# Kernel optimization log

Hardware: AMD Instinct MI355X
Metric: run time of the kernel (lower is better)

Reference implementation:

```python
import jax, jax.numpy as jnp
import numpy as np

KSIZE, SCALE, STRIDE, SOFTMAX_SCALE = 3, 3, 1, 10.0
ESCAPE_NAN = 1e-4
DN = ('NCHW', 'OIHW', 'NCHW')


def same_pad(x, k, stride):
    # torch same_padding: pad so out = ceil(in/stride)
    H, W = x.shape[-2], x.shape[-1]
    oh, ow = -(-H // stride), -(-W // stride)
    ph = max(0, (oh - 1) * stride + k - H)
    pw = max(0, (ow - 1) * stride + k - W)
    return jnp.pad(x, ((0, 0), (0, 0), (ph // 2, ph - ph // 2), (pw // 2, pw - pw // 2)))


def extract_patches(img, k, stride):
    # img [B,C,H,W] already padded -> [B, L, C, k, k], matching torch Unfold ordering (C slowest, kh, kw)
    B, C, H, W = img.shape
    oh, ow = (H - k) // stride + 1, (W - k) // stride + 1
    cols = [img[:, :, i:i + stride * oh:stride, j:j + stride * ow:stride]
            for i in range(k) for j in range(k)]
    p = jnp.stack(cols, axis=2)                      # [B, C, k*k, oh, ow]
    p = p.reshape(B, C, k, k, oh * ow)               # [B, C, k, k, L]
    return jnp.transpose(p, (0, 4, 1, 2, 3))         # [B, L, C, k, k]


def conv1x1_prelu(x, W, b, a):
    y = jnp.einsum('bchw,oc->bohw', x, W) + b[None, :, None, None]
    return jnp.where(y >= 0, y, a * y)


def bilinear_down(x, Ho, Wo):
    # F.interpolate(mode='bilinear', align_corners=False), no antialias
    H, W = x.shape[-2], x.shape[-1]
    def coords(o, s):
        src = (jnp.arange(o, dtype=jnp.float32) + 0.5) * (s / o) - 0.5
        src = jnp.clip(src, 0.0, s - 1.0)
        i0 = jnp.floor(src).astype(jnp.int32)
        i1 = jnp.minimum(i0 + 1, s - 1)
        return i0, i1, src - i0.astype(jnp.float32)
    y0, y1, wy = coords(Ho, H)
    x0, x1, wx = coords(Wo, W)
    r = x[:, :, y0, :] * (1.0 - wy)[:, None] + x[:, :, y1, :] * wy[:, None]
    return r[:, :, :, x0] * (1.0 - wx) + r[:, :, :, x1] * wx


def forward(x, Wa, ba, aa, Wm1, bm1, am1, Wm2, bm2, am2):
    B, C, H, W = x.shape
    kernel = SCALE * KSIZE  # 9
    embed_w = conv1x1_prelu(x, Wa, ba, aa)      # [B,C,H,W]
    match = conv1x1_prelu(x, Wm1, bm1, am1)     # [B,C/2,H,W]
    # large-scale patches used as conv_transpose kernels: [B, L, C, 9, 9]
    raw_w = extract_patches(same_pad(embed_w, kernel, STRIDE * SCALE), kernel, STRIDE * SCALE)
    Hr, Wr = H // SCALE, W // SCALE
    ref = conv1x1_prelu(bilinear_down(x, Hr, Wr), Wm2, bm2, am2)  # [B,C/2,Hr,Wr]
    # small-scale patches used as correlation kernels: [B, L, C/2, 3, 3]
    w = extract_patches(same_pad(ref, KSIZE, STRIDE), KSIZE, STRIDE)
    norm = jnp.sqrt(jnp.sum(w * w, axis=(2, 3, 4), keepdims=True))
    wn = w / jnp.maximum(norm, ESCAPE_NAN)
    xp = same_pad(match, KSIZE, 1)  # [B,C/2,H+2,W+2]

    def corr(xi, wi):  # xi [C/2,H+2,W+2], wi [L,C/2,3,3] -> [L,H,W]
        return jax.lax.conv_general_dilated(xi[None], wi, (1, 1), 'VALID', dimension_numbers=DN)[0]

    y = jax.vmap(corr)(xp, wn)                  # [B,L,H,W]
    y = jax.nn.softmax(y * SOFTMAX_SCALE, axis=1)

    pad = kernel - 1 - SCALE  # conv_transpose2d(stride=3, padding=3) equivalent padding = 5

    def tconv(yi, rwi):  # yi [L,H,W], rwi [L,C,9,9] -> [C,3H,3W]
        k = jnp.transpose(jnp.flip(rwi, (-2, -1)), (1, 0, 2, 3))  # [C,L,9,9]
        return jax.lax.conv_general_dilated(
            yi[None], k, (1, 1), [(pad, pad), (pad, pad)],
            lhs_dilation=(STRIDE * SCALE, STRIDE * SCALE), dimension_numbers=DN)[0]

    out = jax.vmap(tconv)(y, raw_w) / 6.0       # [B,C,3H,3W]
    return out


def setup_inputs() -> dict:
    key = jax.random.key(0)
    ks = jax.random.split(key, 8)
    B, C, H, W = 4, 64, 60, 60
    C2 = C // 2
    return {
        'x': jax.random.normal(ks[0], (B, C, H, W), jnp.float32),
        'Wa': jax.random.normal(ks[1], (C, C), jnp.float32) * 0.1,
        'ba': jax.random.normal(ks[2], (C,), jnp.float32) * 0.1,
        'aa': jnp.full((1,), 0.25, jnp.float32),
        'Wm1': jax.random.normal(ks[3], (C2, C), jnp.float32) * 0.1,
        'bm1': jax.random.normal(ks[4], (C2,), jnp.float32) * 0.1,
        'am1': jnp.full((1,), 0.25, jnp.float32),
        'Wm2': jax.random.normal(ks[5], (C2, C), jnp.float32) * 0.1,
        'bm2': jax.random.normal(ks[6], (C2,), jnp.float32) * 0.1,
        'am2': jnp.full((1,), 0.25, jnp.float32),
    }


def reference(x, Wa, ba, aa, Wm1, bm1, am1, Wm2, bm2, am2):
    return forward(x, Wa, ba, aa, Wm1, bm1, am1, Wm2, bm2, am2)
```

## Files before the change

### kernel.cpp

```cpp
#include <hip/hip_runtime.h>
#include <hip/hip_bf16.h>

typedef __hip_bfloat16 bf16_t;
using f32x4  = __attribute__((ext_vector_type(4))) float;
using bf16x8 = __attribute__((ext_vector_type(8))) short;

#define NB 4
#define NC 64
#define NC2 32
#define NH 60
#define NW 60
#define NPIX (NH*NW)
#define HP 66
#define MP 62
#define HR 20
#define RP 22
#define NL 400
#define OHW 180
#define KPAD 512

#define OFF_XPB   2230272
#define OFF_REFP  3214336
#define OFF_YBL   3462144
#define OFF_AP    14982144
#define OFF_EB    29727744
#define OFF_XP    32087040
#define OFF_RF    40381440

__global__ __launch_bounds__(256) void k_conv(
    const float* __restrict__ x,
    const float* __restrict__ Wa,  const float* __restrict__ ba,  const float* __restrict__ aa,
    const float* __restrict__ Wm1, const float* __restrict__ bm1, const float* __restrict__ am1,
    const float* __restrict__ Wm2, const float* __restrict__ bm2, const float* __restrict__ am2,
    bf16_t* __restrict__ E_bt, bf16_t* __restrict__ xpb, float* __restrict__ refp) {
  int bid = blockIdx.x;
  int t = threadIdx.x;
  if (bid < 300) {
    __shared__ float Ws[64*64];
    __shared__ float bs[64];
    __shared__ float al;
    int b = bid / 75, pblk = bid % 75;
    for (int i = t; i < 64*64; i += 256) {
      int co = i >> 6, c = i & 63;
      Ws[c*64 + co] = Wa[i];
    }
    if (t < 64) bs[t] = ba[t];
    if (t == 0) al = aa[0];
    __syncthreads();
    int lane = t & 63, wid = t >> 6;
    int pix0 = pblk*48 + wid*12;
    const float* xb = x + b*NC*NPIX + pix0;
    float acc[12];
    #pragma unroll
    for (int p = 0; p < 12; ++p) acc[p] = bs[lane];
    for (int c = 0; c < 64; ++c) {
      float wv = Ws[c*64 + lane];
      const float* xc = xb + c*NPIX;
      #pragma unroll
      for (int p = 0; p < 12; ++p)
        acc[p] = fmaf(xc[p], wv, acc[p]);
    }
    #pragma unroll
    for (int p = 0; p < 12; ++p) {
      float v = acc[p];
      v = v >= 0.f ? v : al*v;
      int pix = pix0 + p;
      int ph = pix / NW, pw = pix % NW;
      E_bt[((b*HP + ph+3)*HP + (pw+3))*NC + lane] = __float2bfloat16(v);
    }
  } else if (bid < 2100) {
    int idx = (bid - 300)*256 + t;
    int pix = idx % NPIX; int tmp = idx / NPIX;
    int co = tmp % NC2; int b = tmp / NC2;
    float alpha = am1[0];
    const float* xb = x + b*NC*NPIX + pix;
    const float* wr = Wm1 + co*64;
    float acc = bm1[co];
    #pragma unroll 8
    for (int c = 0; c < 64; ++c)
      acc = fmaf(xb[c*NPIX], wr[c], acc);
    acc = acc >= 0.f ? acc : alpha*acc;
    int ph = pix / NW, pw = pix % NW;
    xpb[((b*NC2 + co)*MP + ph+1)*MP + (pw+1)] = __float2bfloat16(acc);
  } else {
    int idx = (bid - 2100)*256 + t;
    int pos = idx % (HR*HR); int tmp = idx / (HR*HR);
    int co = tmp % NC2; int b = tmp / NC2;
    int hr = pos / HR, wr_ = pos % HR;
    float alpha = am2[0];
    const float* xb = x + b*NC*NPIX + (3*hr+1)*NW + (3*wr_+1);
    const float* wrow = Wm2 + co*64;
    float acc = bm2[co];
    #pragma unroll 8
    for (int c = 0; c < 64; ++c)
      acc = fmaf(xb[c*NPIX], wrow[c], acc);
    acc = acc >= 0.f ? acc : alpha*acc;
    refp[((b*NC2 + co)*RP + hr+1)*RP + (wr_+1)] = acc;
  }
}

__global__ __launch_bounds__(256) void k_swz(
    const bf16_t* __restrict__ xpb, const float* __restrict__ refp,
    const bf16_t* __restrict__ E_bt,
    bf16_t* __restrict__ Xp, bf16_t* __restrict__ Rf, bf16_t* __restrict__ Eb) {
  __shared__ float scl[16];
  int bid = blockIdx.x;
  int t = threadIdx.x;
  if (bid < 2025) {
    int tid = bid*256 + t;
    int slot = tid & 63; int rest = tid >> 6;
    int ks = rest % 9; int rest2 = rest / 9;
    int mblk = rest2 % 225; int b = rest2 / 225;
    int m = mblk*16 + (slot & 15);
    int h = m / NW, w = m % NW;
    int k0 = ks*32 + (slot >> 4)*8;
    const bf16_t* xb = xpb + (size_t)b*NC2*MP*MP;
    union { bf16_t a[8]; bf16x8 v; } u;
    #pragma unroll
    for (int j = 0; j < 8; ++j) {
      int k = k0 + j;
      int c = k / 9, r = k % 9;
      int i = r / 3, j2 = r % 3;
      u.a[j] = xb[(c*MP + h + i)*MP + w + j2];
    }
    *(bf16x8*)(Xp + (size_t)tid*8) = u.v;
  } else if (bid < 2125) {
    int r2 = bid - 2025;
    int nblk = r2 % 25, b = r2 / 25;
    int ll = t >> 4, sub = t & 15;
    int l = nblk*16 + ll;
    int lh = l / HR, lw = l % HR;
    const float* rb = refp + (size_t)b*NC2*RP*RP;
    float ss = 0.f;
    #pragma unroll
    for (int e0 = 0; e0 < 18; ++e0) {
      int e = sub*18 + e0;
      int c = e / 9, r = e % 9;
      int i = r / 3, j = r % 3;
      float v = rb[(c*RP + lh + i)*RP + lw + j];
      ss = fmaf(v, v, ss);
    }
    #pragma unroll
    for (int off = 1; off < 16; off <<= 1)
      ss += __shfl_xor(ss, off);
    if (sub == 0) scl[ll] = 10.f / fmaxf(sqrtf(ss), 1e-4f);
    __syncthreads();
    for (int sidx = t; sidx < 576; sidx += 256) {
      int ks = sidx >> 6, slot = sidx & 63;
      int l2 = nblk*16 + (slot & 15);
      int lh2 = l2 / HR, lw2 = l2 % HR;
      float sc = scl[slot & 15];
      int k0 = ks*32 + (slot >> 4)*8;
      union { bf16_t a[8]; bf16x8 v; } u;
      #pragma unroll
      for (int j = 0; j < 8; ++j) {
        int k = k0 + j;
        int c = k / 9, r = k % 9;
        int i = r / 3, j2 = r % 3;
        u.a[j] = __float2bfloat16(rb[(c*RP + lh2 + i)*RP + lw2 + j2] * sc);
      }
      *(bf16x8*)(Rf + ((size_t)(b*25 + nblk)*576 + sidx)*8) = u.v;
    }
  } else {
    int r2 = bid - 2125;
    int n = r2 % 576, b = r2 / 576;
    int c = n / 9, n9 = n % 9, rr = n9 / 3, s = n9 % 3;
    size_t nbase = ((size_t)(b*12 + n/48)*16);
    const unsigned short* Eu = (const unsigned short*)E_bt;
    unsigned short* Ebu = (unsigned short*)Eb;
    for (int k = t; k < KPAD; k += 256) {
      unsigned short v = 0;
      if (k < 484) {
        int u = k / 22, vv = k % 22;
        v = Eu[((size_t)((b*HP + 3*u + rr)*HP + 3*vv + s))*NC + c];
      }
      size_t idx = (((nbase + (k>>5))*3 + (n%48)/16)*64 + ((k>>3)&3)*16 + (n&15))*8 + (k&7);
      Ebu[idx] = v;
    }
  }
}

__global__ __launch_bounds__(64) void k_cgemm(
    const bf16x8* __restrict__ Xp, const bf16x8* __restrict__ Rf,
    bf16_t* __restrict__ y_bl) {
  int L = threadIdx.x;
  int o = blockIdx.x;
  int xcd = o & 7, sl = o >> 3;
  int w = (xcd < 4 ? xcd*188 : 752 + (xcd-4)*187) + sl;
  int b = w / 375; int rem = w % 375;
  int mt = rem / 5, nt = rem % 5;
  const bf16x8* pa = Xp + ((size_t)(b*225 + mt*3)*9)*64 + L;
  const bf16x8* pb = Rf + ((size_t)(b*25 + nt*5)*9)*64 + L;
  f32x4 acc[3][5];
  #pragma unroll
  for (int i = 0; i < 3; ++i)
    #pragma unroll
    for (int j = 0; j < 5; ++j)
      acc[i][j] = {0.f, 0.f, 0.f, 0.f};
  bf16x8 af[3], bf[5], afn[3], bfn[5];
  #pragma unroll
  for (int i = 0; i < 3; ++i) af[i] = pa[i*576];
  #pragma unroll
  for (int j = 0; j < 5; ++j) bf[j] = pb[j*576];
  for (int ks = 0; ks < 9; ++ks) {
    if (ks < 8) {
      #pragma unroll
      for (int i = 0; i < 3; ++i) afn[i] = pa[i*576 + (ks+1)*64];
      #pragma unroll
      for (int j = 0; j < 5; ++j) bfn[j] = pb[j*576 + (ks+1)*64];
    }
    #pragma unroll
    for (int i = 0; i < 3; ++i)
      #pragma unroll
      for (int j = 0; j < 5; ++j)
        acc[i][j] = __builtin_amdgcn_mfma_f32_16x16x32_bf16(af[i], bf[j], acc[i][j], 0, 0, 0);
    #pragma unroll
    for (int i = 0; i < 3; ++i) af[i] = afn[i];
    #pragma unroll
    for (int j = 0; j < 5; ++j) bf[j] = bfn[j];
  }
  int quad = L >> 4, col = L & 15;
  #pragma unroll
  for (int mf = 0; mf < 3; ++mf) {
    #pragma unroll
    for (int r = 0; r < 4; ++r) {
      int m = mt*48 + mf*16 + quad*4 + r;
      bf16_t* row = y_bl + ((size_t)(b*NPIX + m))*NL + nt*80 + col;
      #pragma unroll
      for (int nf = 0; nf < 5; ++nf)
        row[nf*16] = __float2bfloat16(acc[mf][nf][r]);
    }
  }
}

__device__ __forceinline__ float lo_bf(unsigned int u) {
  return __uint_as_float(u << 16);
}
__device__ __forceinline__ float hi_bf(unsigned int u) {
  return __uint_as_float(u & 0xffff0000u);
}
__device__ __forceinline__ float u16_bf(unsigned short u) {
  return __uint_as_float(((unsigned int)u) << 16);
}
__device__ __forceinline__ unsigned short bf_bits(float f) {
  union { bf16_t h; unsigned short u; } c;
  c.h = __float2bfloat16(f);
  return c.u;
}

__global__ __launch_bounds__(512) void k_saprime(
    const unsigned int* __restrict__ y_b32, bf16_t* __restrict__ Ap) {
  __shared__ uint4 raw[2592];
  unsigned short* ysp = (unsigned short*)raw;
  int t = threadIdx.x;
  int b = blockIdx.z;
  int h0base = blockIdx.y*4, w0base = blockIdx.x*4;
  for (int i = t; i < 2592; i += 512) raw[i] = uint4{0,0,0,0};
  __syncthreads();

  int wave = t >> 6, lane = t & 63;
  bool act = lane < 50;
  for (int pos = wave; pos < 36; pos += 8) {
    int i = pos / 6, jj = pos % 6;
    int hh = h0base - 1 + i, ww = w0base - 1 + jj;
    if (!((unsigned)hh < NH && (unsigned)ww < NW)) continue;
    const uint4* src4 = (const uint4*)(y_b32 + ((size_t)(b*NPIX + hh*NW + ww))*200);
    uint4 v = act ? src4[lane] : uint4{0,0,0,0};
    float f[8];
    if (act) {
      f[0] = lo_bf(v.x); f[1] = hi_bf(v.x);
      f[2] = lo_bf(v.y); f[3] = hi_bf(v.y);
      f[4] = lo_bf(v.z); f[5] = hi_bf(v.z);
      f[6] = lo_bf(v.w); f[7] = hi_bf(v.w);
    } else {
      #pragma unroll
      for (int k = 0; k < 8; ++k) f[k] = -1e30f;
    }
    float m = -1e30f;
    #pragma unroll
    for (int k = 0; k < 8; ++k) m = fmaxf(m, f[k]);
    #pragma unroll
    for (int off = 32; off > 0; off >>= 1)
      m = fmaxf(m, __shfl_xor(m, off));
    float s = 0.f;
    #pragma unroll
    for (int k = 0; k < 8; ++k) {
      float e = __expf(f[k] - m);
      f[k] = e;
      s += e;
    }
    #pragma unroll
    for (int off = 32; off > 0; off >>= 1)
      s += __shfl_xor(s, off);
    float r = 1.f / s;
    if (act) {
      #pragma unroll
      for (int k = 0; k < 4; ++k) {
        int l2 = lane*4 + k;
        int lh = l2 / 10, lw = 2*l2 - 20*lh;
        union { bf16_t h[2]; unsigned int u; } pk;
        pk.h[0] = __float2bfloat16(f[2*k]   * r);
        pk.h[1] = __float2bfloat16(f[2*k+1] * r);
        *(unsigned int*)&ysp[pos*576 + (lh+2)*24 + (lw+2)] = pk.u;
      }
    }
  }
  __syncthreads();

  int row = t >> 5;
  int klane = t & 31;
  int h0r = row >> 2, w0r = row & 3;
  int m = (h0base + h0r)*NW + (w0base + w0r);
  int pblk = m / 80, pf = (m % 80) >> 4, mrow = m & 15;
  size_t rowbase = ((size_t)(b*45 + pblk)*16);
  const unsigned short* basep = ysp + (h0r*6 + w0r)*576;
  unsigned short* Apu = (unsigned short*)Ap;
  for (int kk = 0; kk < 8; ++kk) {
    int k = kk*64 + 2*klane;
    float a0 = 0.f, a1 = 0.f;
    if (k < 484) {
      int u = k / 22, v = k - 22*u;
      const unsigned short* q = basep + u*24 + v;
      #pragma unroll
      for (int dh = 0; dh < 3; ++dh) {
        unsigned int p0 = *(const unsigned int*)(q + dh*3480);
        a0 += lo_bf(p0); a1 += hi_bf(p0);
        a0 += u16_bf(q[dh*3480 + 577]);
        a1 += u16_bf(q[dh*3480 + 578]);
        unsigned int p2 = *(const unsigned int*)(q + dh*3480 + 1154);
        a0 += lo_bf(p2); a1 += hi_bf(p2);
      }
    }
    unsigned int pk = ((unsigned int)bf_bits(a1) << 16) | bf_bits(a0);
    size_t idx = (((rowbase + (k>>5))*5 + pf)*64 + ((k>>3)&3)*16 + mrow)*8 + (k&7);
    *(unsigned int*)&Apu[idx] = pk;
  }
}

__global__ __launch_bounds__(64) void k_tgemm(
    const bf16x8* __restrict__ Eb, const bf16x8* __restrict__ Ap,
    float* __restrict__ out) {
  int L = threadIdx.x;
  int o = blockIdx.x;
  int w = (o & 7)*270 + (o >> 3);
  int b = w / 540; int rem = w % 540;
  int pbi = rem / 12, rb = rem % 12;
  const bf16x8* pa = Eb + ((size_t)(b*12 + rb)*16)*3*64 + L;
  const bf16x8* pp = Ap + ((size_t)(b*45 + pbi)*16)*5*64 + L;
  f32x4 acc[3][5];
  #pragma unroll
  for (int i = 0; i < 3; ++i)
    #pragma unroll
    for (int j = 0; j < 5; ++j)
      acc[i][j] = {0.f, 0.f, 0.f, 0.f};
  bf16x8 af[3], bf[5], afn[3], bfn[5];
  #pragma unroll
  for (int i = 0; i < 3; ++i) af[i] = pa[i*64];
  #pragma unroll
  for (int j = 0; j < 5; ++j) bf[j] = pp[j*64];
  for (int ks = 0; ks < 16; ++ks) {
    if (ks < 15) {
      const bf16x8* na = pa + (ks+1)*192;
      const bf16x8* nb = pp + (ks+1)*320;
      #pragma unroll
      for (int i = 0; i < 3; ++i) afn[i] = na[i*64];
      #pragma unroll
      for (int j = 0; j < 5; ++j) bfn[j] = nb[j*64];
    }
    #pragma unroll
    for (int i = 0; i < 3; ++i)
      #pragma unroll
      for (int j = 0; j < 5; ++j)
        acc[i][j] = __builtin_amdgcn_mfma_f32_16x16x32_bf16(af[i], bf[j], acc[i][j], 0, 0, 0);
    #pragma unroll
    for (int i = 0; i < 3; ++i) af[i] = afn[i];
    #pragma unroll
    for (int j = 0; j < 5; ++j) bf[j] = bfn[j];
  }
  int quad = L >> 4, col = L & 15;
  const float sc = 1.f/6.f;
  #pragma unroll
  for (int pf = 0; pf < 5; ++pf) {
    int m = pbi*80 + pf*16 + col;
    int h0 = m / 60, w0 = m % 60;
    int posoff = b*(NC*OHW*OHW) + h0*540 + w0*3;
    #pragma unroll
    for (int rf = 0; rf < 3; ++rf) {
      #pragma unroll
      for (int r = 0; r < 4; ++r) {
        int n = rb*48 + rf*16 + quad*4 + r;
        int c = n / 9, n9 = n % 9;
        int rr = n9 / 3, s = n9 % 3;
        out[posoff + c*32400 + rr*180 + s] = acc[rf][pf][r] * sc;
      }
    }
  }
}

extern "C" void kernel_launch(void* const* d_in, const int* in_sizes, int n_in,
                              void* d_out, int out_size, void* d_ws, size_t ws_size,
                              hipStream_t stream) {
  (void)in_sizes; (void)n_in; (void)out_size; (void)ws_size;
  const float* x   = (const float*)d_in[0];
  const float* Wa  = (const float*)d_in[1];
  const float* ba  = (const float*)d_in[2];
  const float* aa  = (const float*)d_in[3];
  const float* Wm1 = (const float*)d_in[4];
  const float* bm1 = (const float*)d_in[5];
  const float* am1 = (const float*)d_in[6];
  const float* Wm2 = (const float*)d_in[7];
  const float* bm2 = (const float*)d_in[8];
  const float* am2 = (const float*)d_in[9];
  float* out = (float*)d_out;

  char* base = (char*)d_ws;
  bf16_t* E_bt  = (bf16_t*)base;
  bf16_t* xpb   = (bf16_t*)(base + OFF_XPB);
  float*  refp  = (float*)(base + OFF_REFP);
  bf16_t* y_bl  = (bf16_t*)(base + OFF_YBL);
  bf16_t* ApSwz = (bf16_t*)(base + OFF_AP);
  bf16_t* EbSwz = (bf16_t*)(base + OFF_EB);
  bf16_t* XpSwz = (bf16_t*)(base + OFF_XP);
  bf16_t* RfSwz = (bf16_t*)(base + OFF_RF);

  hipMemsetAsync(d_ws, 0, (size_t)OFF_YBL, stream);

  k_conv<<<2300, 256, 0, stream>>>(x, Wa, ba, aa, Wm1, bm1, am1, Wm2, bm2, am2,
                                   E_bt, xpb, refp);
  k_swz<<<4429, 256, 0, stream>>>(xpb, refp, E_bt, XpSwz, RfSwz, EbSwz);
  k_cgemm<<<1500, 64, 0, stream>>>((const bf16x8*)XpSwz, (const bf16x8*)RfSwz, y_bl);
  k_saprime<<<dim3(15, 15, NB), 512, 0, stream>>>((const unsigned int*)y_bl, ApSwz);
  k_tgemm<<<2160, 64, 0, stream>>>((const bf16x8*)EbSwz, (const bf16x8*)ApSwz, out);
}
```

Before: 168.9 us.

## Fuse all stages into one cooperative persistent kernel with grid syncs

Replaces the memset plus five separate kernel launches with a single cooperative kernel of 256 blocks × 512 threads. Stages (zeroing, 1x1 convs, swizzle, correlation GEMM, softmax/aggregation, transposed-conv GEMM) run as grid-stride loops separated by grid.sync(). This is meant to remove launch overhead and inter-kernel gaps. In exchange it fixes parallelism to 256 blocks, leaves the 64-thread GEMM work mapped onto waves inside larger blocks, and pays for a grid-wide barrier between stages.

```diff
diff --git a/kernel.cpp b/kernel.cpp
--- a/kernel.cpp
+++ b/kernel.cpp
@@ -1,5 +1,8 @@
 #include <hip/hip_runtime.h>
 #include <hip/hip_bf16.h>
+#include <hip/hip_cooperative_groups.h>
+
+namespace cg = cooperative_groups;
 
 typedef __hip_bfloat16 bf16_t;
 using f32x4  = __attribute__((ext_vector_type(4))) float;
@@ -27,212 +30,6 @@
 #define OFF_XP    32087040
 #define OFF_RF    40381440
 
-__global__ __launch_bounds__(256) void k_conv(
-    const float* __restrict__ x,
-    const float* __restrict__ Wa,  const float* __restrict__ ba,  const float* __restrict__ aa,
-    const float* __restrict__ Wm1, const float* __restrict__ bm1, const float* __restrict__ am1,
-    const float* __restrict__ Wm2, const float* __restrict__ bm2, const float* __restrict__ am2,
-    bf16_t* __restrict__ E_bt, bf16_t* __restrict__ xpb, float* __restrict__ refp) {
-  int bid = blockIdx.x;
-  int t = threadIdx.x;
-  if (bid < 300) {
-    __shared__ float Ws[64*64];
-    __shared__ float bs[64];
-    __shared__ float al;
-    int b = bid / 75, pblk = bid % 75;
-    for (int i = t; i < 64*64; i += 256) {
-      int co = i >> 6, c = i & 63;
-      Ws[c*64 + co] = Wa[i];
-    }
-    if (t < 64) bs[t] = ba[t];
-    if (t == 0) al = aa[0];
-    __syncthreads();
-    int lane = t & 63, wid = t >> 6;
-    int pix0 = pblk*48 + wid*12;
-    const float* xb = x + b*NC*NPIX + pix0;
-    float acc[12];
-    #pragma unroll
-    for (int p = 0; p < 12; ++p) acc[p] = bs[lane];
-    for (int c = 0; c < 64; ++c) {
-      float wv = Ws[c*64 + lane];
-      const float* xc = xb + c*NPIX;
-      #pragma unroll
-      for (int p = 0; p < 12; ++p)
-        acc[p] = fmaf(xc[p], wv, acc[p]);
-    }
-    #pragma unroll
-    for (int p = 0; p < 12; ++p) {
-      float v = acc[p];
-      v = v >= 0.f ? v : al*v;
-      int pix = pix0 + p;
-      int ph = pix / NW, pw = pix % NW;
-      E_bt[((b*HP + ph+3)*HP + (pw+3))*NC + lane] = __float2bfloat16(v);
-    }
-  } else if (bid < 2100) {
-    int idx = (bid - 300)*256 + t;
-    int pix = idx % NPIX; int tmp = idx / NPIX;
-    int co = tmp % NC2; int b = tmp / NC2;
-    float alpha = am1[0];
-    const float* xb = x + b*NC*NPIX + pix;
-    const float* wr = Wm1 + co*64;
-    float acc = bm1[co];
-    #pragma unroll 8
-    for (int c = 0; c < 64; ++c)
-      acc = fmaf(xb[c*NPIX], wr[c], acc);
-    acc = acc >= 0.f ? acc : alpha*acc;
-    int ph = pix / NW, pw = pix % NW;
-    xpb[((b*NC2 + co)*MP + ph+1)*MP + (pw+1)] = __float2bfloat16(acc);
-  } else {
-    int idx = (bid - 2100)*256 + t;
-    int pos = idx % (HR*HR); int tmp = idx / (HR*HR);
-    int co = tmp % NC2; int b = tmp / NC2;
-    int hr = pos / HR, wr_ = pos % HR;
-    float alpha = am2[0];
-    const float* xb = x + b*NC*NPIX + (3*hr+1)*NW + (3*wr_+1);
-    const float* wrow = Wm2 + co*64;
-    float acc = bm2[co];
-    #pragma unroll 8
-    for (int c = 0; c < 64; ++c)
-      acc = fmaf(xb[c*NPIX], wrow[c], acc);
-    acc = acc >= 0.f ? acc : alpha*acc;
-    refp[((b*NC2 + co)*RP + hr+1)*RP + (wr_+1)] = acc;
-  }
-}
-
-__global__ __launch_bounds__(256) void k_swz(
-    const bf16_t* __restrict__ xpb, const float* __restrict__ refp,
-    const bf16_t* __restrict__ E_bt,
-    bf16_t* __restrict__ Xp, bf16_t* __restrict__ Rf, bf16_t* __restrict__ Eb) {
-  __shared__ float scl[16];
-  int bid = blockIdx.x;
-  int t = threadIdx.x;
-  if (bid < 2025) {
-    int tid = bid*256 + t;
-    int slot = tid & 63; int rest = tid >> 6;
-    int ks = rest % 9; int rest2 = rest / 9;
-    int mblk = rest2 % 225; int b = rest2 / 225;
-    int m = mblk*16 + (slot & 15);
-    int h = m / NW, w = m % NW;
-    int k0 = ks*32 + (slot >> 4)*8;
-    const bf16_t* xb = xpb + (size_t)b*NC2*MP*MP;
-    union { bf16_t a[8]; bf16x8 v; } u;
-    #pragma unroll
-    for (int j = 0; j < 8; ++j) {
-      int k = k0 + j;
-      int c = k / 9, r = k % 9;
-      int i = r / 3, j2 = r % 3;
-      u.a[j] = xb[(c*MP + h + i)*MP + w + j2];
-    }
-    *(bf16x8*)(Xp + (size_t)tid*8) = u.v;
-  } else if (bid < 2125) {
-    int r2 = bid - 2025;
-    int nblk = r2 % 25, b = r2 / 25;
-    int ll = t >> 4, sub = t & 15;
-    int l = nblk*16 + ll;
-    int lh = l / HR, lw = l % HR;
-    const float* rb = refp + (size_t)b*NC2*RP*RP;
-    float ss = 0.f;
-    #pragma unroll
-    for (int e0 = 0; e0 < 18; ++e0) {
-      int e = sub*18 + e0;
-      int c = e / 9, r = e % 9;
-      int i = r / 3, j = r % 3;
-      float v = rb[(c*RP + lh + i)*RP + lw + j];
-      ss = fmaf(v, v, ss);
-    }
-    #pragma unroll
-    for (int off = 1; off < 16; off <<= 1)
-      ss += __shfl_xor(ss, off);
-    if (sub == 0) scl[ll] = 10.f / fmaxf(sqrtf(ss), 1e-4f);
-    __syncthreads();
-    for (int sidx = t; sidx < 576; sidx += 256) {
-      int ks = sidx >> 6, slot = sidx & 63;
-      int l2 = nblk*16 + (slot & 15);
-      int lh2 = l2 / HR, lw2 = l2 % HR;
-      float sc = scl[slot & 15];
-      int k0 = ks*32 + (slot >> 4)*8;
-      union { bf16_t a[8]; bf16x8 v; } u;
-      #pragma unroll
-      for (int j = 0; j < 8; ++j) {
-        int k = k0 + j;
-        int c = k / 9, r = k % 9;
-        int i = r / 3, j2 = r % 3;
-        u.a[j] = __float2bfloat16(rb[(c*RP + lh2 + i)*RP + lw2 + j2] * sc);
-      }
-      *(bf16x8*)(Rf + ((size_t)(b*25 + nblk)*576 + sidx)*8) = u.v;
-    }
-  } else {
-    int r2 = bid - 2125;
-    int n = r2 % 576, b = r2 / 576;
-    int c = n / 9, n9 = n % 9, rr = n9 / 3, s = n9 % 3;
-    size_t nbase = ((size_t)(b*12 + n/48)*16);
-    const unsigned short* Eu = (const unsigned short*)E_bt;
-    unsigned short* Ebu = (unsigned short*)Eb;
-    for (int k = t; k < KPAD; k += 256) {
-      unsigned short v = 0;
-      if (k < 484) {
-        int u = k / 22, vv = k % 22;
-        v = Eu[((size_t)((b*HP + 3*u + rr)*HP + 3*vv + s))*NC + c];
-      }
-      size_t idx = (((nbase + (k>>5))*3 + (n%48)/16)*64 + ((k>>3)&3)*16 + (n&15))*8 + (k&7);
-      Ebu[idx] = v;
-    }
-  }
-}
-
-__global__ __launch_bounds__(64) void k_cgemm(
-    const bf16x8* __restrict__ Xp, const bf16x8* __restrict__ Rf,
-    bf16_t* __restrict__ y_bl) {
-  int L = threadIdx.x;
-  int o = blockIdx.x;
-  int xcd = o & 7, sl = o >> 3;
-  int w = (xcd < 4 ? xcd*188 : 752 + (xcd-4)*187) + sl;
-  int b = w / 375; int rem = w % 375;
-  int mt = rem / 5, nt = rem % 5;
-  const bf16x8* pa = Xp + ((size_t)(b*225 + mt*3)*9)*64 + L;
-  const bf16x8* pb = Rf + ((size_t)(b*25 + nt*5)*9)*64 + L;
-  f32x4 acc[3][5];
-  #pragma unroll
-  for (int i = 0; i < 3; ++i)
-    #pragma unroll
-    for (int j = 0; j < 5; ++j)
-      acc[i][j] = {0.f, 0.f, 0.f, 0.f};
-  bf16x8 af[3], bf[5], afn[3], bfn[5];
-  #pragma unroll
-  for (int i = 0; i < 3; ++i) af[i] = pa[i*576];
-  #pragma unroll
-  for (int j = 0; j < 5; ++j) bf[j] = pb[j*576];
-  for (int ks = 0; ks < 9; ++ks) {
-    if (ks < 8) {
-      #pragma unroll
-      for (int i = 0; i < 3; ++i) afn[i] = pa[i*576 + (ks+1)*64];
-      #pragma unroll
-      for (int j = 0; j < 5; ++j) bfn[j] = pb[j*576 + (ks+1)*64];
-    }
-    #pragma unroll
-    for (int i = 0; i < 3; ++i)
-      #pragma unroll
-      for (int j = 0; j < 5; ++j)
-        acc[i][j] = __builtin_amdgcn_mfma_f32_16x16x32_bf16(af[i], bf[j], acc[i][j], 0, 0, 0);
-    #pragma unroll
-    for (int i = 0; i < 3; ++i) af[i] = afn[i];
-    #pragma unroll
-    for (int j = 0; j < 5; ++j) bf[j] = bfn[j];
-  }
-  int quad = L >> 4, col = L & 15;
-  #pragma unroll
-  for (int mf = 0; mf < 3; ++mf) {
-    #pragma unroll
-    for (int r = 0; r < 4; ++r) {
-      int m = mt*48 + mf*16 + quad*4 + r;
-      bf16_t* row = y_bl + ((size_t)(b*NPIX + m))*NL + nt*80 + col;
-      #pragma unroll
-      for (int nf = 0; nf < 5; ++nf)
-        row[nf*16] = __float2bfloat16(acc[mf][nf][r]);
-    }
-  }
-}
-
 __device__ __forceinline__ float lo_bf(unsigned int u) {
   return __uint_as_float(u << 16);
 }
@@ -248,150 +45,393 @@
   return c.u;
 }
 
-__global__ __launch_bounds__(512) void k_saprime(
-    const unsigned int* __restrict__ y_b32, bf16_t* __restrict__ Ap) {
-  __shared__ uint4 raw[2592];
-  unsigned short* ysp = (unsigned short*)raw;
-  int t = threadIdx.x;
-  int b = blockIdx.z;
-  int h0base = blockIdx.y*4, w0base = blockIdx.x*4;
-  for (int i = t; i < 2592; i += 512) raw[i] = uint4{0,0,0,0};
-  __syncthreads();
-
-  int wave = t >> 6, lane = t & 63;
-  bool act = lane < 50;
-  for (int pos = wave; pos < 36; pos += 8) {
-    int i = pos / 6, jj = pos % 6;
-    int hh = h0base - 1 + i, ww = w0base - 1 + jj;
-    if (!((unsigned)hh < NH && (unsigned)ww < NW)) continue;
-    const uint4* src4 = (const uint4*)(y_b32 + ((size_t)(b*NPIX + hh*NW + ww))*200);
-    uint4 v = act ? src4[lane] : uint4{0,0,0,0};
-    float f[8];
-    if (act) {
-      f[0] = lo_bf(v.x); f[1] = hi_bf(v.x);
-      f[2] = lo_bf(v.y); f[3] = hi_bf(v.y);
-      f[4] = lo_bf(v.z); f[5] = hi_bf(v.z);
-      f[6] = lo_bf(v.w); f[7] = hi_bf(v.w);
-    } else {
-      #pragma unroll
-      for (int k = 0; k < 8; ++k) f[k] = -1e30f;
-    }
-    float m = -1e30f;
-    #pragma unroll
-    for (int k = 0; k < 8; ++k) m = fmaxf(m, f[k]);
-    #pragma unroll
-    for (int off = 32; off > 0; off >>= 1)
-      m = fmaxf(m, __shfl_xor(m, off));
-    float s = 0.f;
-    #pragma unroll
-    for (int k = 0; k < 8; ++k) {
-      float e = __expf(f[k] - m);
-      f[k] = e;
-      s += e;
-    }
-    #pragma unroll
-    for (int off = 32; off > 0; off >>= 1)
-      s += __shfl_xor(s, off);
-    float r = 1.f / s;
-    if (act) {
-      #pragma unroll
-      for (int k = 0; k < 4; ++k) {
-        int l2 = lane*4 + k;
-        int lh = l2 / 10, lw = 2*l2 - 20*lh;
-        union { bf16_t h[2]; unsigned int u; } pk;
-        pk.h[0] = __float2bfloat16(f[2*k]   * r);
-        pk.h[1] = __float2bfloat16(f[2*k+1] * r);
-        *(unsigned int*)&ysp[pos*576 + (lh+2)*24 + (lw+2)] = pk.u;
-      }
-    }
-  }
-  __syncthreads();
-
-  int row = t >> 5;
-  int klane = t & 31;
-  int h0r = row >> 2, w0r = row & 3;
-  int m = (h0base + h0r)*NW + (w0base + w0r);
-  int pblk = m / 80, pf = (m % 80) >> 4, mrow = m & 15;
-  size_t rowbase = ((size_t)(b*45 + pblk)*16);
-  const unsigned short* basep = ysp + (h0r*6 + w0r)*576;
-  unsigned short* Apu = (unsigned short*)Ap;
-  for (int kk = 0; kk < 8; ++kk) {
-    int k = kk*64 + 2*klane;
-    float a0 = 0.f, a1 = 0.f;
-    if (k < 484) {
-      int u = k / 22, v = k - 22*u;
-      const unsigned short* q = basep + u*24 + v;
-      #pragma unroll
-      for (int dh = 0; dh < 3; ++dh) {
-        unsigned int p0 = *(const unsigned int*)(q + dh*3480);
-        a0 += lo_bf(p0); a1 += hi_bf(p0);
-        a0 += u16_bf(q[dh*3480 + 577]);
-        a1 += u16_bf(q[dh*3480 + 578]);
-        unsigned int p2 = *(const unsigned int*)(q + dh*3480 + 1154);
-        a0 += lo_bf(p2); a1 += hi_bf(p2);
-      }
-    }
-    unsigned int pk = ((unsigned int)bf_bits(a1) << 16) | bf_bits(a0);
-    size_t idx = (((rowbase + (k>>5))*5 + pf)*64 + ((k>>3)&3)*16 + mrow)*8 + (k&7);
-    *(unsigned int*)&Apu[idx] = pk;
-  }
-}
-
-__global__ __launch_bounds__(64) void k_tgemm(
-    const bf16x8* __restrict__ Eb, const bf16x8* __restrict__ Ap,
-    float* __restrict__ out) {
-  int L = threadIdx.x;
-  int o = blockIdx.x;
-  int w = (o & 7)*270 + (o >> 3);
-  int b = w / 540; int rem = w % 540;
-  int pbi = rem / 12, rb = rem % 12;
-  const bf16x8* pa = Eb + ((size_t)(b*12 + rb)*16)*3*64 + L;
-  const bf16x8* pp = Ap + ((size_t)(b*45 + pbi)*16)*5*64 + L;
-  f32x4 acc[3][5];
-  #pragma unroll
-  for (int i = 0; i < 3; ++i)
-    #pragma unroll
-    for (int j = 0; j < 5; ++j)
-      acc[i][j] = {0.f, 0.f, 0.f, 0.f};
-  bf16x8 af[3], bf[5], afn[3], bfn[5];
-  #pragma unroll
-  for (int i = 0; i < 3; ++i) af[i] = pa[i*64];
-  #pragma unroll
-  for (int j = 0; j < 5; ++j) bf[j] = pp[j*64];
-  for (int ks = 0; ks < 16; ++ks) {
-    if (ks < 15) {
-      const bf16x8* na = pa + (ks+1)*192;
-      const bf16x8* nb = pp + (ks+1)*320;
-      #pragma unroll
-      for (int i = 0; i < 3; ++i) afn[i] = na[i*64];
-      #pragma unroll
-      for (int j = 0; j < 5; ++j) bfn[j] = nb[j*64];
-    }
-    #pragma unroll
-    for (int i = 0; i < 3; ++i)
-      #pragma unroll
-      for (int j = 0; j < 5; ++j)
-        acc[i][j] = __builtin_amdgcn_mfma_f32_16x16x32_bf16(af[i], bf[j], acc[i][j], 0, 0, 0);
-    #pragma unroll
-    for (int i = 0; i < 3; ++i) af[i] = afn[i];
-    #pragma unroll
-    for (int j = 0; j < 5; ++j) bf[j] = bfn[j];
-  }
-  int quad = L >> 4, col = L & 15;
-  const float sc = 1.f/6.f;
-  #pragma unroll
-  for (int pf = 0; pf < 5; ++pf) {
-    int m = pbi*80 + pf*16 + col;
-    int h0 = m / 60, w0 = m % 60;
-    int posoff = b*(NC*OHW*OHW) + h0*540 + w0*3;
-    #pragma unroll
-    for (int rf = 0; rf < 3; ++rf) {
-      #pragma unroll
-      for (int r = 0; r < 4; ++r) {
-        int n = rb*48 + rf*16 + quad*4 + r;
-        int c = n / 9, n9 = n % 9;
-        int rr = n9 / 3, s = n9 % 3;
-        out[posoff + c*32400 + rr*180 + s] = acc[rf][pf][r] * sc;
+__global__ __launch_bounds__(512) void k_mega(
+    const float* x, const float* Wa, const float* ba, const float* aa,
+    const float* Wm1, const float* bm1, const float* am1,
+    const float* Wm2, const float* bm2, const float* am2,
+    char* ws, float* out) {
+  cg::grid_group grid = cg::this_grid();
+  __shared__ __align__(16) char smraw[41472];
+  const int bid = blockIdx.x;
+  const int t = threadIdx.x;
+
+  bf16_t* E_bt = (bf16_t*)ws;
+  bf16_t* xpb  = (bf16_t*)(ws + OFF_XPB);
+  float*  refp = (float*)(ws + OFF_REFP);
+  bf16_t* y_bl = (bf16_t*)(ws + OFF_YBL);
+  bf16_t* Ap   = (bf16_t*)(ws + OFF_AP);
+  bf16_t* Eb   = (bf16_t*)(ws + OFF_EB);
+  bf16_t* Xp   = (bf16_t*)(ws + OFF_XP);
+  bf16_t* Rf   = (bf16_t*)(ws + OFF_RF);
+
+  {
+    uint4 z = uint4{0u,0u,0u,0u};
+    uint4* wz = (uint4*)ws;
+    for (int i = bid*512 + t; i < OFF_YBL/16; i += 131072) wz[i] = z;
+  }
+  grid.sync();
+
+  {
+    float* Ws  = (float*)smraw;
+    float* bs  = (float*)(smraw + 16384);
+    float* alp = (float*)(smraw + 16640);
+    for (int i = t; i < 64*64; i += 512) {
+      int co = i >> 6, c = i & 63;
+      Ws[c*64 + co] = Wa[i];
+    }
+    if (t < 64) bs[t] = ba[t];
+    if (t == 0) alp[0] = aa[0];
+    __syncthreads();
+    int half = t >> 8, tt = t & 255;
+    for (int u = bid*2 + half; u < 2300; u += 512) {
+      if (u < 300) {
+        int b = u / 75, pblk = u % 75;
+        int lane = tt & 63, wid2 = tt >> 6;
+        int pix0 = pblk*48 + wid2*12;
+        const float* xb = x + b*NC*NPIX + pix0;
+        float acc[12];
+        #pragma unroll
+        for (int p = 0; p < 12; ++p) acc[p] = bs[lane];
+        for (int c = 0; c < 64; ++c) {
+          float wv = Ws[c*64 + lane];
+          const float* xc = xb + c*NPIX;
+          #pragma unroll
+          for (int p = 0; p < 12; ++p)
+            acc[p] = fmaf(xc[p], wv, acc[p]);
+        }
+        float al = alp[0];
+        #pragma unroll
+        for (int p = 0; p < 12; ++p) {
+          float v = acc[p];
+          v = v >= 0.f ? v : al*v;
+          int pix = pix0 + p;
+          int ph = pix / NW, pw = pix % NW;
+          E_bt[((b*HP + ph+3)*HP + (pw+3))*NC + lane] = __float2bfloat16(v);
+        }
+      } else if (u < 2100) {
+        int idx = (u - 300)*256 + tt;
+        int pix = idx % NPIX; int tmp = idx / NPIX;
+        int co = tmp & 31; int b = tmp >> 5;
+        float alpha = am1[0];
+        const float* xb2 = x + b*NC*NPIX + pix;
+        const float* wr = Wm1 + co*64;
+        float acc = bm1[co];
+        #pragma unroll 8
+        for (int c = 0; c < 64; ++c)
+          acc = fmaf(xb2[c*NPIX], wr[c], acc);
+        acc = acc >= 0.f ? acc : alpha*acc;
+        int ph = pix / NW, pw = pix % NW;
+        xpb[((b*NC2 + co)*MP + ph+1)*MP + (pw+1)] = __float2bfloat16(acc);
+      } else {
+        int idx = (u - 2100)*256 + tt;
+        int pos = idx % (HR*HR); int tmp = idx / (HR*HR);
+        int co = tmp & 31; int b = tmp >> 5;
+        int hr = pos / HR, wr_ = pos % HR;
+        float alpha = am2[0];
+        const float* xb2 = x + b*NC*NPIX + (3*hr+1)*NW + (3*wr_+1);
+        const float* wrow = Wm2 + co*64;
+        float acc = bm2[co];
+        #pragma unroll 8
+        for (int c = 0; c < 64; ++c)
+          acc = fmaf(xb2[c*NPIX], wrow[c], acc);
+        acc = acc >= 0.f ? acc : alpha*acc;
+        refp[((b*NC2 + co)*RP + hr+1)*RP + (wr_+1)] = acc;
+      }
+    }
+  }
+  grid.sync();
+
+  {
+    int half = t >> 8, tt = t & 255;
+    for (int uu = bid*2 + half; uu < 4329; uu += 512) {
+      if (uu < 2025) {
+        int tid = uu*256 + tt;
+        int slot = tid & 63; int rest = tid >> 6;
+        int ks = rest % 9; int rest2 = rest / 9;
+        int mblk = rest2 % 225; int b = rest2 / 225;
+        int m = mblk*16 + (slot & 15);
+        int h = m / NW, w = m % NW;
+        int k0 = ks*32 + (slot >> 4)*8;
+        const bf16_t* xb = xpb + (size_t)b*NC2*MP*MP;
+        union { bf16_t a[8]; bf16x8 v; } uv;
+        #pragma unroll
+        for (int j = 0; j < 8; ++j) {
+          int k = k0 + j;
+          int c = k / 9, r = k % 9;
+          int i = r / 3, j2 = r % 3;
+          uv.a[j] = xb[(c*MP + h + i)*MP + w + j2];
+        }
+        *(bf16x8*)(Xp + (size_t)tid*8) = uv.v;
+      } else {
+        int r2 = uu - 2025;
+        int n = r2 % 576, b = r2 / 576;
+        int c = n / 9, n9 = n % 9, rr = n9 / 3, s = n9 % 3;
+        size_t nbase = ((size_t)(b*12 + n/48)*16);
+        const unsigned short* Eu = (const unsigned short*)E_bt;
+        unsigned short* Ebu = (unsigned short*)Eb;
+        for (int k = tt; k < KPAD; k += 256) {
+          unsigned short v = 0;
+          if (k < 484) {
+            int u2 = k / 22, vv = k % 22;
+            v = Eu[((size_t)((b*HP + 3*u2 + rr)*HP + 3*vv + s))*NC + c];
+          }
+          size_t idx = (((nbase + (k>>5))*3 + (n%48)/16)*64 + ((k>>3)&3)*16 + (n&15))*8 + (k&7);
+          Ebu[idx] = v;
+        }
+      }
+    }
+    if (bid < 100) {
+      float* scl = (float*)smraw;
+      int nblk = bid % 25, b = bid / 25;
+      const float* rb = refp + (size_t)b*NC2*RP*RP;
+      if (t < 256) {
+        int ll = t >> 4, sub = t & 15;
+        int l = nblk*16 + ll;
+        int lh = l / HR, lw = l % HR;
+        float ss = 0.f;
+        #pragma unroll
+        for (int e0 = 0; e0 < 18; ++e0) {
+          int e = sub*18 + e0;
+          int c = e / 9, r = e % 9;
+          int i = r / 3, j = r % 3;
+          float v = rb[(c*RP + lh + i)*RP + lw + j];
+          ss = fmaf(v, v, ss);
+        }
+        #pragma unroll
+        for (int off = 1; off < 16; off <<= 1)
+          ss += __shfl_xor(ss, off);
+        if (sub == 0) scl[ll] = 10.f / fmaxf(sqrtf(ss), 1e-4f);
+      }
+      __syncthreads();
+      for (int sidx = t; sidx < 576; sidx += 512) {
+        int ks = sidx >> 6, slot = sidx & 63;
+        int l2 = nblk*16 + (slot & 15);
+        int lh2 = l2 / HR, lw2 = l2 % HR;
+        float sc = scl[slot & 15];
+        int k0 = ks*32 + (slot >> 4)*8;
+        union { bf16_t a[8]; bf16x8 v; } uv;
+        #pragma unroll
+        for (int j = 0; j < 8; ++j) {
+          int k = k0 + j;
+          int c = k / 9, r = k % 9;
+          int i = r / 3, j2 = r % 3;
+          uv.a[j] = __float2bfloat16(rb[(c*RP + lh2 + i)*RP + lw2 + j2] * sc);
+        }
+        *(bf16x8*)(Rf + ((size_t)(b*25 + nblk)*576 + sidx)*8) = uv.v;
+      }
+    }
+  }
+  grid.sync();
+
+  {
+    const bf16x8* Xp8 = (const bf16x8*)Xp;
+    const bf16x8* Rf8 = (const bf16x8*)Rf;
+    int L = t & 63, wid = t >> 6;
+    int xcd = bid & 7, j = bid >> 3;
+    int sl = j*8 + wid;
+    int chunk = (xcd < 4) ? 188 : 187;
+    int start = (xcd < 4) ? xcd*188 : 752 + (xcd-4)*187;
+    if (sl < chunk) {
+      int w = start + sl;
+      int b = w / 375; int rem = w % 375;
+      int mt = rem / 5, nt = rem % 5;
+      const bf16x8* pa = Xp8 + ((size_t)(b*225 + mt*3)*9)*64 + L;
+      const bf16x8* pb = Rf8 + ((size_t)(b*25 + nt*5)*9)*64 + L;
+      f32x4 acc[3][5];
+      #pragma unroll
+      for (int i = 0; i < 3; ++i)
+        #pragma unroll
+        for (int jj = 0; jj < 5; ++jj)
+          acc[i][jj] = {0.f, 0.f, 0.f, 0.f};
+      bf16x8 af[3], bf[5], afn[3], bfn[5];
+      #pragma unroll
+      for (int i = 0; i < 3; ++i) af[i] = pa[i*576];
+      #pragma unroll
+      for (int jj = 0; jj < 5; ++jj) bf[jj] = pb[jj*576];
+      for (int ks = 0; ks < 9; ++ks) {
+        if (ks < 8) {
+          #pragma unroll
+          for (int i = 0; i < 3; ++i) afn[i] = pa[i*576 + (ks+1)*64];
+          #pragma unroll
+          for (int jj = 0; jj < 5; ++jj) bfn[jj] = pb[jj*576 + (ks+1)*64];
+        }
+        #pragma unroll
+        for (int i = 0; i < 3; ++i)
+          #pragma unroll
+          for (int jj = 0; jj < 5; ++jj)
+            acc[i][jj] = __builtin_amdgcn_mfma_f32_16x16x32_bf16(af[i], bf[jj], acc[i][jj], 0, 0, 0);
+        #pragma unroll
+        for (int i = 0; i < 3; ++i) af[i] = afn[i];
+        #pragma unroll
+        for (int jj = 0; jj < 5; ++jj) bf[jj] = bfn[jj];
+      }
+      int quad = L >> 4, col = L & 15;
+      #pragma unroll
+      for (int mf = 0; mf < 3; ++mf) {
+        #pragma unroll
+        for (int r = 0; r < 4; ++r) {
+          int m = mt*48 + mf*16 + quad*4 + r;
+          bf16_t* row = y_bl + ((size_t)(b*NPIX + m))*NL + nt*80 + col;
+          #pragma unroll
+          for (int nf = 0; nf < 5; ++nf)
+            row[nf*16] = __float2bfloat16(acc[mf][nf][r]);
+        }
+      }
+    }
+  }
+  grid.sync();
+
+  {
+    const unsigned int* y_b32 = (const unsigned int*)y_bl;
+    uint4* raw = (uint4*)smraw;
+    unsigned short* ysp = (unsigned short*)smraw;
+    for (int tile = bid; tile < 900; tile += 256) {
+      int b = tile / 225, rest = tile % 225;
+      int h0base = (rest / 15)*4, w0base = (rest % 15)*4;
+      for (int i = t; i < 2592; i += 512) raw[i] = uint4{0u,0u,0u,0u};
+      __syncthreads();
+
+      int wave = t >> 6, lane = t & 63;
+      bool act = lane < 50;
+      for (int pos = wave; pos < 36; pos += 8) {
+        int i = pos / 6, jj = pos % 6;
+        int hh = h0base - 1 + i, ww = w0base - 1 + jj;
+        if (!((unsigned)hh < NH && (unsigned)ww < NW)) continue;
+        const uint4* src4 = (const uint4*)(y_b32 + ((size_t)(b*NPIX + hh*NW + ww))*200);
+        uint4 v = act ? src4[lane] : uint4{0u,0u,0u,0u};
+        float f[8];
+        if (act) {
+          f[0] = lo_bf(v.x); f[1] = hi_bf(v.x);
+          f[2] = lo_bf(v.y); f[3] = hi_bf(v.y);
+          f[4] = lo_bf(v.z); f[5] = hi_bf(v.z);
+          f[6] = lo_bf(v.w); f[7] = hi_bf(v.w);
+        } else {
+          #pragma unroll
+          for (int k = 0; k < 8; ++k) f[k] = -1e30f;
+        }
+        float m = -1e30f;
+        #pragma unroll
+        for (int k = 0; k < 8; ++k) m = fmaxf(m, f[k]);
+        #pragma unroll
+        for (int off = 32; off > 0; off >>= 1)
+          m = fmaxf(m, __shfl_xor(m, off));
+        float s = 0.f;
+        #pragma unroll
+        for (int k = 0; k < 8; ++k) {
+          float e = __expf(f[k] - m);
+          f[k] = e;
+          s += e;
+        }
+        #pragma unroll
+        for (int off = 32; off > 0; off >>= 1)
+          s += __shfl_xor(s, off);
+        float r = 1.f / s;
+        if (act) {
+          #pragma unroll
+          for (int k = 0; k < 4; ++k) {
+            int l2 = lane*4 + k;
+            int lh = l2 / 10, lw = 2*l2 - 20*lh;
+            union { bf16_t h[2]; unsigned int u; } pk;
+            pk.h[0] = __float2bfloat16(f[2*k]   * r);
+            pk.h[1] = __float2bfloat16(f[2*k+1] * r);
+            *(unsigned int*)&ysp[pos*576 + (lh+2)*24 + (lw+2)] = pk.u;
+          }
+        }
+      }
+      __syncthreads();
+
+      int row = t >> 5;
+      int klane = t & 31;
+      int h0r = row >> 2, w0r = row & 3;
+      int m = (h0base + h0r)*NW + (w0base + w0r);
+      int pblk = m / 80, pf = (m % 80) >> 4, mrow = m & 15;
+      size_t rowbase = ((size_t)(b*45 + pblk)*16);
+      const unsigned short* basep = ysp + (h0r*6 + w0r)*576;
+      unsigned short* Apu = (unsigned short*)Ap;
+      for (int kk = 0; kk < 8; ++kk) {
+        int k = kk*64 + 2*klane;
+        float a0 = 0.f, a1 = 0.f;
+        if (k < 484) {
+          int u2 = k / 22, v = k - 22*u2;
+          const unsigned short* q = basep + u2*24 + v;
+          #pragma unroll
+          for (int dh = 0; dh < 3; ++dh) {
+            unsigned int p0 = *(const unsigned int*)(q + dh*3480);
+            a0 += lo_bf(p0); a1 += hi_bf(p0);
+            a0 += u16_bf(q[dh*3480 + 577]);
+            a1 += u16_bf(q[dh*3480 + 578]);
+            unsigned int p2 = *(const unsigned int*)(q + dh*3480 + 1154);
+            a0 += lo_bf(p2); a1 += hi_bf(p2);
+          }
+        }
+        unsigned int pk = ((unsigned int)bf_bits(a1) << 16) | bf_bits(a0);
+        size_t idx = (((rowbase + (k>>5))*5 + pf)*64 + ((k>>3)&3)*16 + mrow)*8 + (k&7);
+        *(unsigned int*)&Apu[idx] = pk;
+      }
+      __syncthreads();
+    }
+  }
+  grid.sync();
+
+  {
+    const bf16x8* Eb8 = (const bf16x8*)Eb;
+    const bf16x8* Ap8 = (const bf16x8*)Ap;
+    int L = t & 63, wid = t >> 6;
+    int xcd = bid & 7, j = bid >> 3;
+    int base_s = j*8 + wid;
+    for (int s2 = base_s; s2 < 270; s2 += 256) {
+      int w = xcd*270 + s2;
+      int b = w / 540; int rem = w % 540;
+      int pbi = rem / 12, rb = rem % 12;
+      const bf16x8* pa = Eb8 + ((size_t)(b*12 + rb)*16)*3*64 + L;
+      const bf16x8* pp = Ap8 + ((size_t)(b*45 + pbi)*16)*5*64 + L;
+      f32x4 acc[3][5];
+      #pragma unroll
+      for (int i = 0; i < 3; ++i)
+        #pragma unroll
+        for (int jj = 0; jj < 5; ++jj)
+          acc[i][jj] = {0.f, 0.f, 0.f, 0.f};
+      bf16x8 af[3], bf[5], afn[3], bfn[5];
+      #pragma unroll
+      for (int i = 0; i < 3; ++i) af[i] = pa[i*64];
+      #pragma unroll
+      for (int jj = 0; jj < 5; ++jj) bf[jj] = pp[jj*64];
+      for (int ks = 0; ks < 16; ++ks) {
+        if (ks < 15) {
+          const bf16x8* na = pa + (ks+1)*192;
+          const bf16x8* nb = pp + (ks+1)*320;
+          #pragma unroll
+          for (int i = 0; i < 3; ++i) afn[i] = na[i*64];
+          #pragma unroll
+          for (int jj = 0; jj < 5; ++jj) bfn[jj] = nb[jj*64];
+        }
+        #pragma unroll
+        for (int i = 0; i < 3; ++i)
+          #pragma unroll
+          for (int jj = 0; jj < 5; ++jj)
+            acc[i][jj] = __builtin_amdgcn_mfma_f32_16x16x32_bf16(af[i], bf[jj], acc[i][jj], 0, 0, 0);
+        #pragma unroll
+        for (int i = 0; i < 3; ++i) af[i] = afn[i];
+        #pragma unroll
+        for (int jj = 0; jj < 5; ++jj) bf[jj] = bfn[jj];
+      }
+      int quad = L >> 4, col = L & 15;
+      const float sc = 1.f/6.f;
+      #pragma unroll
+      for (int pf = 0; pf < 5; ++pf) {
+        int m = pbi*80 + pf*16 + col;
+        int h0 = m / 60, w0 = m % 60;
+        int posoff = b*(NC*OHW*OHW) + h0*540 + w0*3;
+        #pragma unroll
+        for (int rf = 0; rf < 3; ++rf) {
+          #pragma unroll
+          for (int r = 0; r < 4; ++r) {
+            int n = rb*48 + rf*16 + quad*4 + r;
+            int c = n / 9, n9 = n % 9;
+            int rr = n9 / 3, s = n9 % 3;
+            out[posoff + c*32400 + rr*180 + s] = acc[rf][pf][r] * sc;
+          }
+        }
       }
     }
   }
@@ -412,23 +452,10 @@
   const float* bm2 = (const float*)d_in[8];
   const float* am2 = (const float*)d_in[9];
   float* out = (float*)d_out;
-
-  char* base = (char*)d_ws;
-  bf16_t* E_bt  = (bf16_t*)base;
-  bf16_t* xpb   = (bf16_t*)(base + OFF_XPB);
-  float*  refp  = (float*)(base + OFF_REFP);
-  bf16_t* y_bl  = (bf16_t*)(base + OFF_YBL);
-  bf16_t* ApSwz = (bf16_t*)(base + OFF_AP);
-  bf16_t* EbSwz = (bf16_t*)(base + OFF_EB);
-  bf16_t* XpSwz = (bf16_t*)(base + OFF_XP);
-  bf16_t* RfSwz = (bf16_t*)(base + OFF_RF);
-
-  hipMemsetAsync(d_ws, 0, (size_t)OFF_YBL, stream);
-
-  k_conv<<<2300, 256, 0, stream>>>(x, Wa, ba, aa, Wm1, bm1, am1, Wm2, bm2, am2,
-                                   E_bt, xpb, refp);
-  k_swz<<<4429, 256, 0, stream>>>(xpb, refp, E_bt, XpSwz, RfSwz, EbSwz);
-  k_cgemm<<<1500, 64, 0, stream>>>((const bf16x8*)XpSwz, (const bf16x8*)RfSwz, y_bl);
-  k_saprime<<<dim3(15, 15, NB), 512, 0, stream>>>((const unsigned int*)y_bl, ApSwz);
-  k_tgemm<<<2160, 64, 0, stream>>>((const bf16x8*)EbSwz, (const bf16x8*)ApSwz, out);
-}
+  char* wsb = (char*)d_ws;
+
+  void* kargs[] = { &x, &Wa, &ba, &aa, &Wm1, &bm1, &am1,
+                    &Wm2, &bm2, &am2, &wsb, &out };
+  hipLaunchCooperativeKernel((const void*)k_mega, dim3(256), dim3(512),
+                             kargs, 0, stream);
+}
```

New measurement: 377.0 us. 123% more time.
